# Performance work log

Hardware: AMD Instinct MI355X
Metric: run time of the kernel (lower is better)

The kernel has to match this reference:

```python
import jax, jax.numpy as jnp
import numpy as np

D_MODEL = 1024
N_HEAD = 16
HEAD_DIM = D_MODEL // N_HEAD
LN_EPS = 1e-12


def setup_inputs() -> dict:
    key = jax.random.key(0)
    ks = jax.random.split(key, 9)
    B, S, D = 2, 2048, D_MODEL
    s = 1.0 / np.sqrt(D)
    return {
        "hidden_states": jax.random.normal(ks[0], (B, S, D), jnp.float32),
        "Wq": jax.random.normal(ks[1], (D, D), jnp.float32) * s,
        "bq": jnp.zeros((D,), jnp.float32),
        "Wk": jax.random.normal(ks[2], (D, D), jnp.float32) * s,
        "bk": jnp.zeros((D,), jnp.float32),
        "Wv": jax.random.normal(ks[3], (D, D), jnp.float32) * s,
        "bv": jnp.zeros((D,), jnp.float32),
        "Wo": jax.random.normal(ks[4], (D, D), jnp.float32) * s,
        "bo": jnp.zeros((D,), jnp.float32),
        "ln_gamma": jnp.ones((D,), jnp.float32),
        "ln_beta": jnp.zeros((D,), jnp.float32),
    }


def reference(hidden_states, Wq, bq, Wk, bk, Wv, bv, Wo, bo, ln_gamma, ln_beta):
    # BertAttention forward (eval mode: dropouts are identity).
    B, S, D = hidden_states.shape
    H, Dh = N_HEAD, HEAD_DIM

    def heads(x):  # [B,S,D] -> [B,H,S,Dh]
        return x.reshape(B, S, H, Dh).transpose(0, 2, 1, 3)

    q = heads(hidden_states @ Wq + bq)
    k = heads(hidden_states @ Wk + bk)
    v = heads(hidden_states @ Wv + bv)

    scores = jnp.einsum("bhsd,bhtd->bhst", q, k) / jnp.sqrt(jnp.float32(Dh))
    probs = jax.nn.softmax(scores, axis=-1)
    ctx = jnp.einsum("bhst,bhtd->bhsd", probs, v)
    ctx = ctx.transpose(0, 2, 1, 3).reshape(B, S, D)

    # BertSelfOutput: dense + residual + LayerNorm(eps=1e-12)
    h = ctx @ Wo + bo + hidden_states
    mu = jnp.mean(h, axis=-1, keepdims=True)
    var = jnp.mean(jnp.square(h - mu), axis=-1, keepdims=True)
    out = (h - mu) / jnp.sqrt(var + LN_EPS) * ln_gamma + ln_beta
    return out
```

## Files before the change

### kernel.cpp

```cpp
#include <hip/hip_runtime.h>
#include <hip/hip_bf16.h>

#define D_MODEL 1024
#define N_HEAD  16
#define HEAD_DIM 64
#define BATCH   2
#define SEQ     2048
#define M_ROWS  (BATCH * SEQ)

typedef unsigned short u16;
typedef unsigned int   u32;

typedef __attribute__((ext_vector_type(8))) short bfrag8;
typedef __attribute__((ext_vector_type(4))) float ffrag4;

__device__ __forceinline__ float bf2f(u16 u) {
    return __uint_as_float(((u32)u) << 16);
}
__device__ __forceinline__ u16 f2bf(float f) {
    u32 x = __float_as_uint(f);
    u32 r = (x + 0x7fffu + ((x >> 16) & 1u)) >> 16;
    return (u16)r;
}
__device__ __forceinline__ u32 pack_bf2_trunc(float lo, float hi) {
    return __builtin_amdgcn_perm(__float_as_uint(hi), __float_as_uint(lo),
                                 0x07060302u);
}
__device__ __forceinline__ float fast_exp2(float x) {
    float r;
    asm("v_exp_f32 %0, %1" : "=v"(r) : "v"(x));
    return r;
}

__device__ __forceinline__ void gl_lds16(const void* g, void* l) {
    __builtin_amdgcn_global_load_lds(
        (const __attribute__((address_space(1))) void*)g,
        (__attribute__((address_space(3))) void*)l, 16, 0, 0);
}

#define Q_PRESCALE 0.18033688011112042f

__device__ __forceinline__ int is_bf16(const u32* gb) {
    return gb[0] != 0x3F800000u;
}

__global__ __launch_bounds__(256) void prep_all(
    const void* w0, const void* w1, const void* w2, const void* w3,
    u16* t0, u16* t1, u16* t2, u16* t3,
    const void* v0, const void* v1, const void* v2, const void* v3,
    const void* v4, const void* v5, u16* __restrict__ vecs,
    const void* xsrc, u16* __restrict__ xdst, int xquads,
    const u32* __restrict__ gb)
{
    const int isbf = is_bf16(gb);
    const int tid = threadIdx.x;
    const int z = blockIdx.z;

    if (z < 4) {
        __shared__ u16 t[32][33];
        const void* srcs[4] = {w0, w1, w2, w3};
        u16* dsts[4] = {t0, t1, t2, t3};
        const void* src = srcs[z];
        u16* dst = dsts[z];
        const int bx = blockIdx.x * 32;
        const int by = blockIdx.y * 32;
        const int tx = tid & 31;
        const int ty = tid >> 5;
#pragma unroll
        for (int r = 0; r < 4; r++) {
            const int row = by + ty * 4 + r;
            u16 v;
            if (isbf) v = ((const u16*)src)[(size_t)row * D_MODEL + bx + tx];
            else      v = f2bf(((const float*)src)[(size_t)row * D_MODEL + bx + tx]);
            t[tx][ty * 4 + r] = v;
        }
        __syncthreads();
#pragma unroll
        for (int r = 0; r < 4; r++) {
            const int n = bx + ty * 4 + r;
            dst[(size_t)n * D_MODEL + by + tx] = t[ty * 4 + r][tx];
        }
        return;
    }

    const int id = blockIdx.y * 32 + blockIdx.x;
    if (id < 6) {
        const void* srcs[6] = {v0, v1, v2, v3, v4, v5};
        const void* src = srcs[id];
        u16* dst = vecs + (size_t)id * D_MODEL;
        if (isbf) {
            ((ushort4*)dst)[tid] = ((const ushort4*)src)[tid];
        } else {
            float4 v = ((const float4*)src)[tid];
            ushort4 o;
            o.x = f2bf(v.x); o.y = f2bf(v.y); o.z = f2bf(v.z); o.w = f2bf(v.w);
            ((ushort4*)dst)[tid] = o;
        }
        return;
    }
    if (isbf) return;
    const int nblk = 32 * 32 - 6;
    for (int i = (id - 6) * 256 + tid; i < xquads; i += nblk * 256) {
        float4 v = ((const float4*)xsrc)[i];
        ushort4 o;
        o.x = f2bf(v.x); o.y = f2bf(v.y); o.z = f2bf(v.z); o.w = f2bf(v.w);
        ((ushort4*)xdst)[i] = o;
    }
}

__global__ __launch_bounds__(256) void qkv_mfma(
    const u16* __restrict__ Xraw, const u16* __restrict__ Xconv,
    const u32* __restrict__ gb,
    const u16* __restrict__ WqT, const u16* __restrict__ bq,
    const u16* __restrict__ WkT, const u16* __restrict__ bk,
    const u16* __restrict__ WvT, const u16* __restrict__ bv,
    u16* __restrict__ Qout, u16* __restrict__ Kout, u16* __restrict__ Vout)
{
    const u16* X = is_bf16(gb) ? Xraw : Xconv;
    const int which = blockIdx.z;
    const u16* Wt   = (which == 0) ? WqT : (which == 1) ? WkT : WvT;
    const u16* bias = (which == 0) ? bq  : (which == 1) ? bk  : bv;
    u16* Out        = (which == 0) ? Qout : (which == 1) ? Kout : Vout;

    __shared__ __align__(16) u16 SMEM[128 * 32 * 2];
    u16* As = SMEM;
    u16* Bs = SMEM + 128 * 32;

    const int tid  = threadIdx.x;
    const int wave = tid >> 6;
    const int lane = tid & 63;
    const int quad = lane >> 4;
    const int l16  = lane & 15;
    const int m0 = blockIdx.y * 128;
    const int n0 = blockIdx.x * 128;
    const int wr = (wave >> 1) * 64;
    const int wc = (wave & 1) * 64;

    ffrag4 acc[4][4];
#pragma unroll
    for (int i = 0; i < 4; i++)
#pragma unroll
        for (int j = 0; j < 4; j++) acc[i][j] = (ffrag4){0.f, 0.f, 0.f, 0.f};

    const int srow  = wave * 32 + (lane >> 2);
    const int scolb = (lane & 3) * 16;
    const char* Xg = (const char*)X  + (size_t)(m0 + srow) * (D_MODEL * 2) + scolb;
    const char* Wg = (const char*)Wt + (size_t)(n0 + srow) * (D_MODEL * 2) + scolb;
    char* lA = (char*)As + wave * 2048;
    char* lB = (char*)Bs + wave * 2048;
    const size_t rstep16 = (size_t)16 * (D_MODEL * 2);

    for (int k0 = 0; k0 < D_MODEL; k0 += 32) {
        __syncthreads();
        gl_lds16(Xg + (size_t)k0 * 2,           lA);
        gl_lds16(Xg + (size_t)k0 * 2 + rstep16, lA + 1024);
        gl_lds16(Wg + (size_t)k0 * 2,           lB);
        gl_lds16(Wg + (size_t)k0 * 2 + rstep16, lB + 1024);
        __syncthreads();

        bfrag8 af[4], bf[4];
#pragma unroll
        for (int mi = 0; mi < 4; mi++)
            af[mi] = *(const bfrag8*)((const char*)As + (wr + mi * 16 + l16) * 64 + quad * 16);
#pragma unroll
        for (int ni = 0; ni < 4; ni++)
            bf[ni] = *(const bfrag8*)((const char*)Bs + (wc + ni * 16 + l16) * 64 + quad * 16);
#pragma unroll
        for (int mi = 0; mi < 4; mi++)
#pragma unroll
            for (int ni = 0; ni < 4; ni++)
                acc[mi][ni] = __builtin_amdgcn_mfma_f32_16x16x32_bf16(
                    af[mi], bf[ni], acc[mi][ni], 0, 0, 0);
    }

    __syncthreads();

    if (which == 2) {
#pragma unroll
        for (int mi = 0; mi < 4; mi++) {
            const int mbase = m0 + wr + mi * 16 + quad * 4;
            const int b = mbase >> 11;
            const int s = mbase & 2047;
#pragma unroll
            for (int ni = 0; ni < 4; ni++) {
                const int n = n0 + wc + ni * 16 + l16;
                const float bia = bf2f(bias[n]);
                ushort4 o;
                o.x = f2bf(acc[mi][ni][0] + bia);
                o.y = f2bf(acc[mi][ni][1] + bia);
                o.z = f2bf(acc[mi][ni][2] + bia);
                o.w = f2bf(acc[mi][ni][3] + bia);
                *(ushort4*)&Out[((size_t)(b * N_HEAD * HEAD_DIM + n)) * SEQ + s] = o;
            }
        }
    } else {
        u16* T = SMEM + wave * (16 * 72);
        const int hh = (n0 + wc) >> 6;
#pragma unroll
        for (int mi = 0; mi < 4; mi++) {
#pragma unroll
            for (int ni = 0; ni < 4; ni++) {
                const int col = ni * 16 + l16;
                const float bia = bf2f(bias[n0 + wc + col]);
#pragma unroll
                for (int r = 0; r < 4; r++) {
                    float v = acc[mi][ni][r] + bia;
                    if (which == 0) v *= Q_PRESCALE;
                    T[(quad * 4 + r) * 72 + col] = f2bf(v);
                }
            }
            asm volatile("s_waitcnt lgkmcnt(0)" ::: "memory");
            const int m = m0 + wr + mi * 16 + l16;
            const int b = m >> 11;
            const int s = m & 2047;
            u16* drow = Out + ((size_t)(b * N_HEAD + hh) * SEQ + s) * HEAD_DIM;
#pragma unroll
            for (int j = 0; j < 2; j++) {
                const int c = j * 32 + quad * 8;
                uint4 v = *(const uint4*)&T[l16 * 72 + c];
                *(uint4*)&drow[c] = v;
            }
        }
    }
}

__global__ __launch_bounds__(256, 2) void attn_mfma(
    const u16* __restrict__ Q, const u16* __restrict__ K,
    const u16* __restrict__ VT, u16* __restrict__ CTX)
{
    __shared__ __align__(16) u16 Ks[2][4096];
    __shared__ __align__(16) u16 Vs[2][4096];
    __shared__ __align__(16) u16 PQ[8192];

    const int tid  = threadIdx.x;
    const int wave = tid >> 6;
    const int lane = tid & 63;
    const int quad = lane >> 4;
    const int l16  = lane & 15;
    const int l7   = l16 & 7;

    const int b  = blockIdx.z;
    const int h  = blockIdx.y;
    const int q0 = blockIdx.x * 128;

    const size_t headoff = (size_t)(b * N_HEAD + h) * SEQ * HEAD_DIM;
    const u16* Qb  = Q  + headoff;
    const u16* Kb  = K  + headoff;
    const u16* VTb = VT + headoff;

    const int srow = tid >> 2;
    const int sc0  = (tid & 3) * 2;
    const int sd0  = srow * 64 + (((sc0    ) ^ (srow & 7)) << 3);
    const int sd1  = srow * 64 + (((sc0 + 1) ^ (srow & 7)) << 3);

    uint4 ka0 = *(const uint4*)&Kb[(size_t)srow * HEAD_DIM + sc0 * 8];
    uint4 ka1 = *(const uint4*)&Kb[(size_t)srow * HEAD_DIM + sc0 * 8 + 8];
    uint4 va0 = *(const uint4*)&VTb[(size_t)srow * SEQ + sc0 * 8];
    uint4 va1 = *(const uint4*)&VTb[(size_t)srow * SEQ + sc0 * 8 + 8];

    {
        const int qrow = tid >> 1;
        const int qcb  = (tid & 1) * 4;
#pragma unroll
        for (int i = 0; i < 4; i++) {
            uint4 v = *(const uint4*)&Qb[(size_t)(q0 + qrow) * HEAD_DIM + (qcb + i) * 8];
            *(uint4*)&PQ[qrow * 64 + (((qcb + i) ^ (qrow & 7)) << 3)] = v;
        }
    }
    __syncthreads();

    const int wq = wave * 32;
    bfrag8 qa[2][2];
#pragma unroll
    for (int g = 0; g < 2; g++)
#pragma unroll
        for (int ch = 0; ch < 2; ch++)
            qa[g][ch] = *(const bfrag8*)&PQ[(wq + g * 16 + l16) * 64 +
                                            (((ch * 4 + quad) ^ l7) << 3)];
    u16* Pw = &PQ[wave * 2048];

    ffrag4 oacc[2][4];
#pragma unroll
    for (int g = 0; g < 2; g++)
#pragma unroll
        for (int c = 0; c < 4; c++) oacc[g][c] = (ffrag4){0.f, 0.f, 0.f, 0.f};
    float lsum[2] = {0.f, 0.f};

    for (int t0 = 0; t0 < SEQ; t0 += 64) {
        const int buf = (t0 >> 6) & 1;
        u16* Kl = Ks[buf];
        u16* Vl = Vs[buf];
        *(uint4*)&Kl[sd0] = ka0;
        *(uint4*)&Kl[sd1] = ka1;
        *(uint4*)&Vl[sd0] = va0;
        *(uint4*)&Vl[sd1] = va1;
        __syncthreads();

        const int tn = (t0 + 64) & (SEQ - 1);
        ka0 = *(const uint4*)&Kb[(size_t)(tn + srow) * HEAD_DIM + sc0 * 8];
        ka1 = *(const uint4*)&Kb[(size_t)(tn + srow) * HEAD_DIM + sc0 * 8 + 8];
        va0 = *(const uint4*)&VTb[(size_t)srow * SEQ + tn + sc0 * 8];
        va1 = *(const uint4*)&VTb[(size_t)srow * SEQ + tn + sc0 * 8 + 8];

        ffrag4 st[4][2];
        __builtin_amdgcn_s_setprio(1);
#pragma unroll
        for (int c = 0; c < 4; c++) {
            const int kr = (c * 16 + l16) * 64;
            const bfrag8 kb0 = *(const bfrag8*)&Kl[kr + ((quad ^ l7) << 3)];
            const bfrag8 kb1 = *(const bfrag8*)&Kl[kr + (((4 + quad) ^ l7) << 3)];
#pragma unroll
            for (int g = 0; g < 2; g++) {
                ffrag4 a = (ffrag4){0.f, 0.f, 0.f, 0.f};
                a = __builtin_amdgcn_mfma_f32_16x16x32_bf16(kb0, qa[g][0], a, 0, 0, 0);
                a = __builtin_amdgcn_mfma_f32_16x16x32_bf16(kb1, qa[g][1], a, 0, 0, 0);
                st[c][g] = a;
            }
        }
        __builtin_amdgcn_s_setprio(0);

#pragma unroll
        for (int g = 0; g < 2; g++) {
            float part = 0.f;
#pragma unroll
            for (int c = 0; c < 4; c++) {
                const float e0 = fast_exp2(st[c][g][0]);
                const float e1 = fast_exp2(st[c][g][1]);
                const float e2 = fast_exp2(st[c][g][2]);
                const float e3 = fast_exp2(st[c][g][3]);
                part += (e0 + e1) + (e2 + e3);
                uint2 pk;
                pk.x = pack_bf2_trunc(e0, e1);
                pk.y = pack_bf2_trunc(e2, e3);
                const int chunk = 2 * c + (quad >> 1);
                *(uint2*)&Pw[(g * 16 + l16) * 64 + ((chunk ^ l7) << 3) +
                             (quad & 1) * 4] = pk;
            }
            part += __shfl_xor(part, 16);
            part += __shfl_xor(part, 32);
            lsum[g] += part;
        }

        asm volatile("s_waitcnt lgkmcnt(0)" ::: "memory");

        bfrag8 pa[2][2];
#pragma unroll
        for (int g = 0; g < 2; g++)
#pragma unroll
            for (int ch = 0; ch < 2; ch++)
                pa[g][ch] = *(const bfrag8*)&Pw[(g * 16 + l16) * 64 +
                                                (((ch * 4 + quad) ^ l7) << 3)];
        __builtin_amdgcn_s_setprio(1);
#pragma unroll
        for (int c = 0; c < 4; c++) {
            const int vr = (c * 16 + l16) * 64;
            const bfrag8 vb0 = *(const bfrag8*)&Vl[vr + ((quad ^ l7) << 3)];
            const bfrag8 vb1 = *(const bfrag8*)&Vl[vr + (((4 + quad) ^ l7) << 3)];
#pragma unroll
            for (int g = 0; g < 2; g++) {
                oacc[g][c] = __builtin_amdgcn_mfma_f32_16x16x32_bf16(pa[g][0], vb0, oacc[g][c], 0, 0, 0);
                oacc[g][c] = __builtin_amdgcn_mfma_f32_16x16x32_bf16(pa[g][1], vb1, oacc[g][c], 0, 0, 0);
            }
        }
        __builtin_amdgcn_s_setprio(0);
    }

#pragma unroll
    for (int g = 0; g < 2; g++) {
        float linv[4];
#pragma unroll
        for (int r = 0; r < 4; r++)
            linv[r] = 1.0f / __shfl(lsum[g], quad * 4 + r, 16);
#pragma unroll
        for (int c = 0; c < 4; c++) {
#pragma unroll
            for (int r = 0; r < 4; r++) {
                const int row = q0 + wq + g * 16 + quad * 4 + r;
                const int dh  = c * 16 + l16;
                CTX[(size_t)(b * SEQ + row) * D_MODEL + h * HEAD_DIM + dh] =
                    f2bf(oacc[g][c][r] * linv[r]);
            }
        }
    }
}

__global__ __launch_bounds__(256) void out_proj_mfma(
    const u16* __restrict__ CTX, const u16* __restrict__ WoT,
    const u16* __restrict__ bo, const u16* __restrict__ Xraw,
    const u16* __restrict__ Xconv, const u32* __restrict__ gb,
    u16* __restrict__ H)
{
    const u16* X = is_bf16(gb) ? Xraw : Xconv;
    __shared__ __align__(16) u16 SMEM[128 * 32 + 64 * 32];
    u16* As = SMEM;
    u16* Bs = SMEM + 128 * 32;

    const int tid  = threadIdx.x;
    const int wave = tid >> 6;
    const int lane = tid & 63;
    const int quad = lane >> 4;
    const int l16  = lane & 15;
    const int m0 = blockIdx.y * 128;
    const int n0 = blockIdx.x * 64;
    const int wr = (wave >> 1) * 64;
    const int wc = (wave & 1) * 32;

    ffrag4 acc[4][2];
#pragma unroll
    for (int i = 0; i < 4; i++)
#pragma unroll
        for (int j = 0; j < 2; j++) acc[i][j] = (ffrag4){0.f, 0.f, 0.f, 0.f};

    const int srowA = wave * 32 + (lane >> 2);
    const int srowB = wave * 16 + (lane >> 2);
    const int scolb = (lane & 3) * 16;
    const char* Ag = (const char*)CTX + (size_t)(m0 + srowA) * (D_MODEL * 2) + scolb;
    const char* Wg = (const char*)WoT + (size_t)(n0 + srowB) * (D_MODEL * 2) + scolb;
    char* lA = (char*)As + wave * 2048;
    char* lB = (char*)Bs + wave * 1024;
    const size_t rstep16 = (size_t)16 * (D_MODEL * 2);

    for (int k0 = 0; k0 < D_MODEL; k0 += 32) {
        __syncthreads();
        gl_lds16(Ag + (size_t)k0 * 2,           lA);
        gl_lds16(Ag + (size_t)k0 * 2 + rstep16, lA + 1024);
        gl_lds16(Wg + (size_t)k0 * 2,           lB);
        __syncthreads();

        bfrag8 af[4], bf[2];
#pragma unroll
        for (int mi = 0; mi < 4; mi++)
            af[mi] = *(const bfrag8*)((const char*)As + (wr + mi * 16 + l16) * 64 + quad * 16);
#pragma unroll
        for (int ni = 0; ni < 2; ni++)
            bf[ni] = *(const bfrag8*)((const char*)Bs + (wc + ni * 16 + l16) * 64 + quad * 16);
#pragma unroll
        for (int mi = 0; mi < 4; mi++)
#pragma unroll
            for (int ni = 0; ni < 2; ni++)
                acc[mi][ni] = __builtin_amdgcn_mfma_f32_16x16x32_bf16(
                    af[mi], bf[ni], acc[mi][ni], 0, 0, 0);
    }

    __syncthreads();

    float* T = (float*)SMEM + wave * (16 * 36);
#pragma unroll
    for (int mi = 0; mi < 4; mi++) {
#pragma unroll
        for (int ni = 0; ni < 2; ni++) {
            const int col = ni * 16 + l16;
#pragma unroll
            for (int r = 0; r < 4; r++)
                T[(quad * 4 + r) * 36 + col] = acc[mi][ni][r];
        }
        asm volatile("s_waitcnt lgkmcnt(0)" ::: "memory");
        const int m = m0 + wr + mi * 16 + l16;
        const int c = quad * 8;
        float4 v0 = *(const float4*)&T[l16 * 36 + c];
        float4 v1 = *(const float4*)&T[l16 * 36 + c + 4];
        const int n = n0 + wc + c;
        ushort4 b0 = *(const ushort4*)&bo[n];
        ushort4 b1 = *(const ushort4*)&bo[n + 4];
        ushort4 x0 = *(const ushort4*)&X[(size_t)m * D_MODEL + n];
        ushort4 x1 = *(const ushort4*)&X[(size_t)m * D_MODEL + n + 4];
        u16 o0 = f2bf(v0.x + bf2f(b0.x) + bf2f(x0.x));
        u16 o1 = f2bf(v0.y + bf2f(b0.y) + bf2f(x0.y));
        u16 o2 = f2bf(v0.z + bf2f(b0.z) + bf2f(x0.z));
        u16 o3 = f2bf(v0.w + bf2f(b0.w) + bf2f(x0.w));
        u16 o4 = f2bf(v1.x + bf2f(b1.x) + bf2f(x1.x));
        u16 o5 = f2bf(v1.y + bf2f(b1.y) + bf2f(x1.y));
        u16 o6 = f2bf(v1.z + bf2f(b1.z) + bf2f(x1.z));
        u16 o7 = f2bf(v1.w + bf2f(b1.w) + bf2f(x1.w));
        uint4 ov;
        ov.x = (u32)o0 | ((u32)o1 << 16);
        ov.y = (u32)o2 | ((u32)o3 << 16);
        ov.z = (u32)o4 | ((u32)o5 << 16);
        ov.w = (u32)o6 | ((u32)o7 << 16);
        *(uint4*)&H[(size_t)m * D_MODEL + n] = ov;
    }
}

__global__ __launch_bounds__(256) void ln_kernel(
    const u16* __restrict__ H, const u16* __restrict__ gamma,
    const u16* __restrict__ beta, void* __restrict__ out,
    const u32* __restrict__ gb)
{
    const int isbf = is_bf16(gb);
    const int row = blockIdx.x;
    const int tid = threadIdx.x;
    const u16* hr = H + (size_t)row * D_MODEL;

    ushort4 hv = *(const ushort4*)&hr[tid * 4];
    float v0 = bf2f(hv.x), v1 = bf2f(hv.y), v2 = bf2f(hv.z), v3 = bf2f(hv.w);
    float s  = (v0 + v1) + (v2 + v3);
    float ss = (v0 * v0 + v1 * v1) + (v2 * v2 + v3 * v3);

#pragma unroll
    for (int off = 1; off < 64; off <<= 1) {
        s  += __shfl_xor(s, off);
        ss += __shfl_xor(ss, off);
    }
    __shared__ float sbuf[4], ssbuf[4];
    const int w = tid >> 6;
    if ((tid & 63) == 0) { sbuf[w] = s; ssbuf[w] = ss; }
    __syncthreads();
    s  = sbuf[0] + sbuf[1] + sbuf[2] + sbuf[3];
    ss = ssbuf[0] + ssbuf[1] + ssbuf[2] + ssbuf[3];

    const float mu  = s * (1.f / D_MODEL);
    const float var = ss * (1.f / D_MODEL) - mu * mu;
    const float inv = rsqrtf(var + 1e-12f);

    const int n = tid * 4;
    ushort4 g4 = *(const ushort4*)&gamma[n];
    ushort4 b4 = *(const ushort4*)&beta[n];
    float o0 = (v0 - mu) * inv * bf2f(g4.x) + bf2f(b4.x);
    float o1 = (v1 - mu) * inv * bf2f(g4.y) + bf2f(b4.y);
    float o2 = (v2 - mu) * inv * bf2f(g4.z) + bf2f(b4.z);
    float o3 = (v3 - mu) * inv * bf2f(g4.w) + bf2f(b4.w);

    if (isbf) {
        ushort4 ov;
        ov.x = f2bf(o0); ov.y = f2bf(o1); ov.z = f2bf(o2); ov.w = f2bf(o3);
        *(ushort4*)&((u16*)out)[(size_t)row * D_MODEL + n] = ov;
    } else {
        *(float4*)&((float*)out)[(size_t)row * D_MODEL + n] =
            make_float4(o0, o1, o2, o3);
    }
}

extern "C" void kernel_launch(void* const* d_in, const int* in_sizes, int n_in,
                              void* d_out, int out_size, void* d_ws, size_t ws_size,
                              hipStream_t stream) {
    const size_t NTOK = (size_t)M_ROWS * D_MODEL;
    const size_t NW   = (size_t)D_MODEL * D_MODEL;
    const size_t NV   = D_MODEL;

    char* wp = (char*)d_ws;
    u16* Xc   = (u16*)wp;                 wp += NTOK * 2;
    u16* WqT  = (u16*)wp;                 wp += NW * 2;
    u16* WkT  = (u16*)wp;                 wp += NW * 2;
    u16* WvT  = (u16*)wp;                 wp += NW * 2;
    u16* WoT  = (u16*)wp;                 wp += NW * 2;
    u16* vecs = (u16*)wp;                 wp += 6 * NV * 2;
    u16* Q    = (u16*)wp;                 wp += NTOK * 2;
    u16* Kt   = (u16*)wp;                 wp += NTOK * 2;
    u16* Vt   = (u16*)wp;                 wp += NTOK * 2;
    u16* H    = Q;
    u16* CTX  = (u16*)d_out;

    u16* bqc = vecs + 0 * NV;
    u16* bkc = vecs + 1 * NV;
    u16* bvc = vecs + 2 * NV;
    u16* boc = vecs + 3 * NV;
    u16* gc  = vecs + 4 * NV;
    u16* bc  = vecs + 5 * NV;

    const u16* Xraw = (const u16*)d_in[0];
    const u32* gb   = (const u32*)d_in[9];

    prep_all<<<dim3(32, 32, 5), 256, 0, stream>>>(
        d_in[1], d_in[3], d_in[5], d_in[7], WqT, WkT, WvT, WoT,
        d_in[2], d_in[4], d_in[6], d_in[8], d_in[9], d_in[10], vecs,
        d_in[0], Xc, (int)(NTOK / 4), gb);

    qkv_mfma<<<dim3(D_MODEL / 128, M_ROWS / 128, 3), 256, 0, stream>>>(
        Xraw, Xc, gb, WqT, bqc, WkT, bkc, WvT, bvc, Q, Kt, Vt);
    attn_mfma<<<dim3(SEQ / 128, N_HEAD, BATCH), 256, 0, stream>>>(Q, Kt, Vt, CTX);
    out_proj_mfma<<<dim3(D_MODEL / 64, M_ROWS / 128), 256, 0, stream>>>(
        CTX, WoT, boc, Xraw, Xc, gb, H);
    ln_kernel<<<M_ROWS, 256, 0, stream>>>(H, gc, bc, d_out, gb);
}
```

Baseline: 223.3 us.

## Fuse Q/K/V projections into one block sharing X tile with smaller 64x64 tiles

Replaces the three-way grid split (one z-slice per Q/K/V) with a single kernel where each block loads one X tile and three weight tiles, computing all three projections from the shared A fragments. Tile size drops from 128x128 to 64x64 per projection, the block count rises, and launch bounds now request 4 blocks per CU. This cuts redundant X loads and should improve occupancy, but each block does less MFMA work per LDS load, so arithmetic intensity per weight tile is lower.

```diff
diff --git a/kernel.cpp b/kernel.cpp
--- a/kernel.cpp
+++ b/kernel.cpp
@@ -108,7 +108,7 @@
     }
 }
 
-__global__ __launch_bounds__(256) void qkv_mfma(
+__global__ __launch_bounds__(256, 4) void qkv_mfma(
     const u16* __restrict__ Xraw, const u16* __restrict__ Xconv,
     const u32* __restrict__ gb,
     const u16* __restrict__ WqT, const u16* __restrict__ bq,
@@ -117,109 +117,109 @@
     u16* __restrict__ Qout, u16* __restrict__ Kout, u16* __restrict__ Vout)
 {
     const u16* X = is_bf16(gb) ? Xraw : Xconv;
-    const int which = blockIdx.z;
-    const u16* Wt   = (which == 0) ? WqT : (which == 1) ? WkT : WvT;
-    const u16* bias = (which == 0) ? bq  : (which == 1) ? bk  : bv;
-    u16* Out        = (which == 0) ? Qout : (which == 1) ? Kout : Vout;
-
-    __shared__ __align__(16) u16 SMEM[128 * 32 * 2];
-    u16* As = SMEM;
-    u16* Bs = SMEM + 128 * 32;
+
+    __shared__ __align__(16) u16 SMEM[64 * 32 * 4];
 
     const int tid  = threadIdx.x;
     const int wave = tid >> 6;
     const int lane = tid & 63;
     const int quad = lane >> 4;
     const int l16  = lane & 15;
-    const int m0 = blockIdx.y * 128;
-    const int n0 = blockIdx.x * 128;
-    const int wr = (wave >> 1) * 64;
-    const int wc = (wave & 1) * 64;
-
-    ffrag4 acc[4][4];
-#pragma unroll
-    for (int i = 0; i < 4; i++)
-#pragma unroll
-        for (int j = 0; j < 4; j++) acc[i][j] = (ffrag4){0.f, 0.f, 0.f, 0.f};
-
-    const int srow  = wave * 32 + (lane >> 2);
+    const int m0 = blockIdx.y * 64;
+    const int n0 = blockIdx.x * 64;
+    const int wr = (wave >> 1) * 32;
+    const int wc = (wave & 1) * 32;
+
+    ffrag4 acc[3][2][2];
+#pragma unroll
+    for (int z = 0; z < 3; z++)
+#pragma unroll
+        for (int i = 0; i < 2; i++)
+#pragma unroll
+            for (int j = 0; j < 2; j++) acc[z][i][j] = (ffrag4){0.f, 0.f, 0.f, 0.f};
+
+    const int srow  = wave * 16 + (lane >> 2);
     const int scolb = (lane & 3) * 16;
-    const char* Xg = (const char*)X  + (size_t)(m0 + srow) * (D_MODEL * 2) + scolb;
-    const char* Wg = (const char*)Wt + (size_t)(n0 + srow) * (D_MODEL * 2) + scolb;
-    char* lA = (char*)As + wave * 2048;
-    char* lB = (char*)Bs + wave * 2048;
-    const size_t rstep16 = (size_t)16 * (D_MODEL * 2);
+    const char* Ag  = (const char*)X   + (size_t)(m0 + srow) * (D_MODEL * 2) + scolb;
+    const char* Bg0 = (const char*)WqT + (size_t)(n0 + srow) * (D_MODEL * 2) + scolb;
+    const char* Bg1 = (const char*)WkT + (size_t)(n0 + srow) * (D_MODEL * 2) + scolb;
+    const char* Bg2 = (const char*)WvT + (size_t)(n0 + srow) * (D_MODEL * 2) + scolb;
+    char* lA  = (char*)SMEM + wave * 1024;
+    char* lB0 = (char*)SMEM + 4096  + wave * 1024;
+    char* lB1 = (char*)SMEM + 8192  + wave * 1024;
+    char* lB2 = (char*)SMEM + 12288 + wave * 1024;
 
     for (int k0 = 0; k0 < D_MODEL; k0 += 32) {
         __syncthreads();
-        gl_lds16(Xg + (size_t)k0 * 2,           lA);
-        gl_lds16(Xg + (size_t)k0 * 2 + rstep16, lA + 1024);
-        gl_lds16(Wg + (size_t)k0 * 2,           lB);
-        gl_lds16(Wg + (size_t)k0 * 2 + rstep16, lB + 1024);
+        gl_lds16(Ag  + (size_t)k0 * 2, lA);
+        gl_lds16(Bg0 + (size_t)k0 * 2, lB0);
+        gl_lds16(Bg1 + (size_t)k0 * 2, lB1);
+        gl_lds16(Bg2 + (size_t)k0 * 2, lB2);
         __syncthreads();
 
-        bfrag8 af[4], bf[4];
-#pragma unroll
-        for (int mi = 0; mi < 4; mi++)
-            af[mi] = *(const bfrag8*)((const char*)As + (wr + mi * 16 + l16) * 64 + quad * 16);
-#pragma unroll
-        for (int ni = 0; ni < 4; ni++)
-            bf[ni] = *(const bfrag8*)((const char*)Bs + (wc + ni * 16 + l16) * 64 + quad * 16);
-#pragma unroll
-        for (int mi = 0; mi < 4; mi++)
-#pragma unroll
-            for (int ni = 0; ni < 4; ni++)
-                acc[mi][ni] = __builtin_amdgcn_mfma_f32_16x16x32_bf16(
-                    af[mi], bf[ni], acc[mi][ni], 0, 0, 0);
+        bfrag8 af[2];
+#pragma unroll
+        for (int mi = 0; mi < 2; mi++)
+            af[mi] = *(const bfrag8*)((const char*)SMEM +
+                       (wr + mi * 16 + l16) * 64 + quad * 16);
+#pragma unroll
+        for (int z = 0; z < 3; z++) {
+            const char* Bz = (const char*)SMEM + 4096 + z * 4096;
+            bfrag8 b0 = *(const bfrag8*)(Bz + (wc      + l16) * 64 + quad * 16);
+            bfrag8 b1 = *(const bfrag8*)(Bz + (wc + 16 + l16) * 64 + quad * 16);
+            acc[z][0][0] = __builtin_amdgcn_mfma_f32_16x16x32_bf16(af[0], b0, acc[z][0][0], 0, 0, 0);
+            acc[z][0][1] = __builtin_amdgcn_mfma_f32_16x16x32_bf16(af[0], b1, acc[z][0][1], 0, 0, 0);
+            acc[z][1][0] = __builtin_amdgcn_mfma_f32_16x16x32_bf16(af[1], b0, acc[z][1][0], 0, 0, 0);
+            acc[z][1][1] = __builtin_amdgcn_mfma_f32_16x16x32_bf16(af[1], b1, acc[z][1][1], 0, 0, 0);
+        }
     }
 
     __syncthreads();
 
-    if (which == 2) {
-#pragma unroll
-        for (int mi = 0; mi < 4; mi++) {
-            const int mbase = m0 + wr + mi * 16 + quad * 4;
-            const int b = mbase >> 11;
-            const int s = mbase & 2047;
-#pragma unroll
-            for (int ni = 0; ni < 4; ni++) {
-                const int n = n0 + wc + ni * 16 + l16;
-                const float bia = bf2f(bias[n]);
-                ushort4 o;
-                o.x = f2bf(acc[mi][ni][0] + bia);
-                o.y = f2bf(acc[mi][ni][1] + bia);
-                o.z = f2bf(acc[mi][ni][2] + bia);
-                o.w = f2bf(acc[mi][ni][3] + bia);
-                *(ushort4*)&Out[((size_t)(b * N_HEAD * HEAD_DIM + n)) * SEQ + s] = o;
-            }
-        }
-    } else {
-        u16* T = SMEM + wave * (16 * 72);
-        const int hh = (n0 + wc) >> 6;
-#pragma unroll
-        for (int mi = 0; mi < 4; mi++) {
-#pragma unroll
-            for (int ni = 0; ni < 4; ni++) {
+    const int h = n0 >> 6;
+    u16* T = SMEM + wave * (16 * 48);
+#pragma unroll
+    for (int z = 0; z < 2; z++) {
+        const u16* bias = (z == 0) ? bq : bk;
+        u16* Out        = (z == 0) ? Qout : Kout;
+#pragma unroll
+        for (int mi = 0; mi < 2; mi++) {
+#pragma unroll
+            for (int ni = 0; ni < 2; ni++) {
                 const int col = ni * 16 + l16;
                 const float bia = bf2f(bias[n0 + wc + col]);
 #pragma unroll
                 for (int r = 0; r < 4; r++) {
-                    float v = acc[mi][ni][r] + bia;
-                    if (which == 0) v *= Q_PRESCALE;
-                    T[(quad * 4 + r) * 72 + col] = f2bf(v);
+                    float v = acc[z][mi][ni][r] + bia;
+                    if (z == 0) v *= Q_PRESCALE;
+                    T[(quad * 4 + r) * 48 + col] = f2bf(v);
                 }
             }
             asm volatile("s_waitcnt lgkmcnt(0)" ::: "memory");
             const int m = m0 + wr + mi * 16 + l16;
             const int b = m >> 11;
             const int s = m & 2047;
-            u16* drow = Out + ((size_t)(b * N_HEAD + hh) * SEQ + s) * HEAD_DIM;
-#pragma unroll
-            for (int j = 0; j < 2; j++) {
-                const int c = j * 32 + quad * 8;
-                uint4 v = *(const uint4*)&T[l16 * 72 + c];
-                *(uint4*)&drow[c] = v;
-            }
+            u16* dst = Out + ((size_t)(b * N_HEAD + h) * SEQ + s) * HEAD_DIM
+                           + wc + quad * 8;
+            *(uint4*)dst = *(const uint4*)&T[l16 * 48 + quad * 8];
+        }
+    }
+
+#pragma unroll
+    for (int mi = 0; mi < 2; mi++) {
+        const int mbase = m0 + wr + mi * 16 + quad * 4;
+        const int b = mbase >> 11;
+        const int s = mbase & 2047;
+#pragma unroll
+        for (int ni = 0; ni < 2; ni++) {
+            const int n = n0 + wc + ni * 16 + l16;
+            const float bia = bf2f(bv[n]);
+            ushort4 o;
+            o.x = f2bf(acc[2][mi][ni][0] + bia);
+            o.y = f2bf(acc[2][mi][ni][1] + bia);
+            o.z = f2bf(acc[2][mi][ni][2] + bia);
+            o.w = f2bf(acc[2][mi][ni][3] + bia);
+            *(ushort4*)&Vout[((size_t)(b * N_HEAD * HEAD_DIM + n)) * SEQ + s] = o;
         }
     }
 }
@@ -565,7 +565,7 @@
         d_in[2], d_in[4], d_in[6], d_in[8], d_in[9], d_in[10], vecs,
         d_in[0], Xc, (int)(NTOK / 4), gb);
 
-    qkv_mfma<<<dim3(D_MODEL / 128, M_ROWS / 128, 3), 256, 0, stream>>>(
+    qkv_mfma<<<dim3(D_MODEL / 64, M_ROWS / 64), 256, 0, stream>>>(
         Xraw, Xc, gb, WqT, bqc, WkT, bkc, WvT, bvc, Q, Kt, Vt);
     attn_mfma<<<dim3(SEQ / 128, N_HEAD, BATCH), 256, 0, stream>>>(Q, Kt, Vt, CTX);
     out_proj_mfma<<<dim3(D_MODEL / 64, M_ROWS / 128), 256, 0, stream>>>(
```

Measured after the change: 212.0 us. -5.0%, faster.
